# Kernel tuning notes

Hardware: AMD Instinct MI355X
Metric: run time of the kernel (lower is better)

## Reference

```python
import jax, jax.numpy as jnp
import numpy as np

N_PART = 32
DIM = 256
BATCH = 8192
N_TRAIN = 8192
EPS = 1e-8


def rbf_kernel(x):
    # x: [n, d] particles; RBF kernel with median heuristic (Liu & Wang SVGD)
    n = x.shape[0]
    sq = jnp.sum(x * x, axis=1)
    pd = sq[:, None] - 2.0 * (x @ x.T) + sq[None, :]          # [n, n] squared dists
    h = jnp.median(pd) / jnp.log(n + 1.0)                      # bandwidth
    kxy = jnp.exp(-pd / h)                                     # [n, n]
    sumk = jnp.sum(kxy, axis=1)
    # sum_j grad_{x_j} k(x_j, x_i): (x_i * sum_j k_ij - sum_j k_ij x_j) * 2/h
    dxkxy = (x * sumk[:, None] - kxy @ x) * (2.0 / h)          # [n, d]
    return kxy, dxkxy


def setup_inputs() -> dict:
    key = jax.random.key(0)
    k1, k2, k3 = jax.random.split(key, 3)
    X = jax.random.normal(k1, (BATCH, DIM), dtype=jnp.float32)
    y = (jax.random.uniform(k2, (BATCH,), dtype=jnp.float32) > 0.5).astype(jnp.float32)
    W = jax.random.uniform(k3, (N_PART, DIM), dtype=jnp.float32) * 0.2 - 0.1
    return {"X": X, "y": y, "W": W}


def reference(X, y, W):
    z = W @ X.T
    p = jax.nn.sigmoid(z)
    denom = p - p * p + EPS
    # dz * dy, where dy = (y - p)/denom and dz = p(1-p)
    dzdy = (p * (1.0 - p)) * (y[None, :] - p) / denom          # [n, B]
    dW = (dzdy @ X) / BATCH                                     # mean over batch -> [n, d]
    # grad_loglik_W = -(dz*dy)[:, :, None] * X[None]  -> [n, B, d]
    glW = (-dzdy)[:, :, None] * X[None, :, :]
    mean_dW = jnp.mean(glW, axis=0)                             # [B, d]
    diff = glW - mean_dW[None]                                  # [n, B, d]
    # mean over particles of diff^T diff, divided by batch_size
    cov = jnp.einsum('nbd,nbe->de', diff, diff) / (N_PART * BATCH)  # [d, d]
    W_grads = dW * N_TRAIN - W                                  # [n, d]
    y_pred = jnp.mean(p, axis=0)                                # [B]
    ll = jnp.mean(y * jnp.log(y_pred + 1e-3) + (1.0 - y) * jnp.log(1.0 - y_pred + 1e-3))
    acc = jnp.mean(((y > 0.5) == (y_pred > 0.5)).astype(jnp.float32))
    # step == 1 -> rho = 0 -> updated cov buffer equals cov
    H_inv = jnp.linalg.inv(cov + 0.01 * jnp.eye(DIM, dtype=cov.dtype))
    kxy, dxkxy = rbf_kernel(W)
    svgd_grad = (kxy @ W_grads + dxkxy) / N_PART               # [n, d]
    kfac_grad = svgd_grad @ H_inv                               # [n, d]
    return (ll, acc, svgd_grad, kfac_grad)
```

## Files before the change

### kernel.cpp

```cpp
#include <hip/hip_runtime.h>

#define NPART 32
#define DIM   256
#define BATCH 8192

#define OFF_S     0u
#define OFF_DWP   270336u
#define OFF_WG    2367488u
#define OFF_COVP  2375680u
#define OFF_H     6569984u
#define OFF_EA    6635520u
#define OFF_EB    6701056u
#define OFF_XA    6766592u
#define OFF_XB    6832128u
#define OFF_SVGD  6897664u
#define OFF_LLP   6905856u
#define OFF_ACCP  6906368u
#define OFF_TAU   6906624u
#define OFF_KXY   6906628u
#define OFF_SUMK  6907652u
#define OFF_HB    6907684u

__device__ __forceinline__ float dot4(float4 a, float4 b) {
  return a.x*b.x + a.y*b.y + a.z*b.z + a.w*b.w;
}

__global__ __launch_bounds__(512) void k_stage1(
    const float4* __restrict__ X4, const float* __restrict__ y,
    const float* __restrict__ W, float* __restrict__ ws)
{
  __shared__ __align__(16) float smemf[17856];
  const int t = threadIdx.x, blk = blockIdx.x;

  float* s_ws = ws + OFF_S;
  double* llp = (double*)(ws + OFF_LLP);
  float* accp = ws + OFF_ACCP;

  if (blk > 0) {
    float2* Wl2 = (float2*)smemf;
    float4* Xl  = (float4*)(smemf + 8384);
    float*  dzl = smemf + 16704;
    double* llred  = (double*)(smemf + 17760);
    float*  accred = smemf + 17824;
    const int chunk = blk - 1;
    const int base = chunk*32;
    const float4* W4g = (const float4*)W;

    #pragma unroll
    for (int i = 0; i < 4; ++i) {
      int idx = t + i*512;
      float4 v = W4g[idx];
      int n = idx >> 6, j = idx & 63;
      Wl2[n*131 + 2*j]     = make_float2(v.x, v.y);
      Wl2[n*131 + 2*j + 1] = make_float2(v.z, v.w);
    }
    #pragma unroll
    for (int i = 0; i < 4; ++i) {
      int idx = t + i*512;
      Xl[(idx>>6)*65 + (idx&63)] = X4[(base + (idx>>6))*64 + (idx&63)];
    }
    __syncthreads();

    const int n = t & 31, b2 = t >> 5;
    float z0 = 0.f, z1 = 0.f;
    #pragma unroll 8
    for (int c = 0; c < 64; ++c) {
      float2 wa = Wl2[n*131 + 2*c], wb = Wl2[n*131 + 2*c + 1];
      float4 xa = Xl[b2*65 + c], xb = Xl[(b2+16)*65 + c];
      z0 += wa.x*xa.x + wa.y*xa.y + wb.x*xa.z + wb.y*xa.w;
      z1 += wa.x*xb.x + wa.y*xb.y + wb.x*xb.z + wb.y*xb.w;
    }
    const int g0 = base + b2, g1 = base + b2 + 16;
    const float y0 = y[g0], y1 = y[g1];
    float p0 = 1.f/(1.f + expf(-z0)), p1 = 1.f/(1.f + expf(-z1));

    auto dzf = [](float p, float yv) {
      float pq = p - p*p;
      return pq*(yv - p)/(pq + 1e-8f);
    };
    float dz0 = dzf(p0, y0), dz1 = dzf(p1, y1);

    float sp0 = p0, sp1 = p1, sd0 = dz0, sd1 = dz1;
    #pragma unroll
    for (int m = 16; m >= 1; m >>= 1) {
      sp0 += __shfl_xor(sp0, m); sp1 += __shfl_xor(sp1, m);
      sd0 += __shfl_xor(sd0, m); sd1 += __shfl_xor(sd1, m);
    }
    const float m0 = sd0*(1.f/32.f), m1 = sd1*(1.f/32.f);
    float q0 = (dz0 - m0)*(dz0 - m0);
    float q1 = (dz1 - m1)*(dz1 - m1);
    #pragma unroll
    for (int m = 16; m >= 1; m >>= 1) {
      q0 += __shfl_xor(q0, m); q1 += __shfl_xor(q1, m);
    }

    dzl[b2*33 + n]      = dz0;
    dzl[(b2+16)*33 + n] = dz1;

    if (n == 0) {
      s_ws[g0] = q0; s_ws[g1] = q1;
      float yp0 = sp0*(1.f/32.f), yp1 = sp1*(1.f/32.f);
      llred[b2]    = (double)(y0*logf(yp0+1e-3f) + (1.f-y0)*logf(1.f-yp0+1e-3f));
      llred[b2+16] = (double)(y1*logf(yp1+1e-3f) + (1.f-y1)*logf(1.f-yp1+1e-3f));
      accred[b2]    = ((y0 > 0.5f) == (yp0 > 0.5f)) ? 1.f : 0.f;
      accred[b2+16] = ((y1 > 0.5f) == (yp1 > 0.5f)) ? 1.f : 0.f;
    }
    __syncthreads();

    const int n2 = t >> 4, c = t & 15;
    float4 acc[4];
    #pragma unroll
    for (int m = 0; m < 4; ++m) acc[m] = make_float4(0.f,0.f,0.f,0.f);
    #pragma unroll 4
    for (int b = 0; b < 32; ++b) {
      float dzv = dzl[b*33 + n2];
      #pragma unroll
      for (int m = 0; m < 4; ++m) {
        float4 xv = Xl[b*65 + c + 16*m];
        acc[m].x += dzv*xv.x; acc[m].y += dzv*xv.y;
        acc[m].z += dzv*xv.z; acc[m].w += dzv*xv.w;
      }
    }
    float4* dWp4 = (float4*)(ws + OFF_DWP);
    #pragma unroll
    for (int m = 0; m < 4; ++m)
      dWp4[chunk*2048 + n2*64 + c + 16*m] = acc[m];

    if (t == 0) {
      double L = 0.0;
      for (int i = 0; i < 32; ++i) L += llred[i];
      llp[chunk] = L;
    } else if (t == 1) {
      float A = 0.f;
      for (int i = 0; i < 32; ++i) A += accred[i];
      accp[chunk] = A;
    }
  } else {
    if (t == 0) *(unsigned*)(ws + OFF_TAU) = 0u;
    float* Wf = &smemf[0];
    float* pd = &smemf[8320];
    float* sb = &smemf[9344];
    for (int i = t; i < 8192; i += 512)
      Wf[(i>>8)*260 + (i&255)] = W[i];
    __syncthreads();
    for (int pp = t; pp < 1024; pp += 512) {
      int i = pp >> 5, j = pp & 31;
      const float4* wa = (const float4*)&Wf[i*260];
      const float4* wb = (const float4*)&Wf[j*260];
      float d2 = 0.f;
      #pragma unroll 8
      for (int c = 0; c < 64; ++c) {
        float4 a = wa[c], b = wb[c];
        float dx=a.x-b.x, dy=a.y-b.y, dz=a.z-b.z, dw=a.w-b.w;
        d2 += dx*dx + dy*dy + dz*dz + dw*dw;
      }
      pd[pp] = d2; sb[pp] = d2;
    }
    __syncthreads();
    for (int k = 2; k <= 1024; k <<= 1) {
      for (int j = k >> 1; j > 0; j >>= 1) {
        #pragma unroll 1
        for (int m = t; m < 1024; m += 512) {
          int ixj = m ^ j;
          if (ixj > m) {
            float a = sb[m], b = sb[ixj];
            bool up = ((m & k) == 0);
            if ((a > b) == up) { sb[m] = b; sb[ixj] = a; }
          }
        }
        __syncthreads();
      }
    }
    const float h = 0.5f*(sb[511] + sb[512]) / logf(33.0f);
    __syncthreads();
    float* kxy = ws + OFF_KXY;
    for (int pp = t; pp < 1024; pp += 512) {
      float kv = expf(-pd[pp]/h);
      sb[pp] = kv;
      kxy[pp] = kv;
    }
    __syncthreads();
    if (t < 32) {
      float s = 0.f;
      #pragma unroll
      for (int j = 0; j < 32; ++j) s += sb[t*32 + j];
      (ws + OFF_SUMK)[t] = s;
    }
    if (t == 0) (ws + OFF_HB)[0] = h;
  }
}

__global__ __launch_bounds__(256) void k_stage2(
    const float4* __restrict__ X4, const float* __restrict__ W,
    float* __restrict__ out, float* __restrict__ ws)
{
  __shared__ __align__(16) float smemf[8448];
  const int t = threadIdx.x, blk = blockIdx.x;
  float* s_ws = ws + OFF_S;
  float* covp = ws + OFF_COVP;

  if (blk == 0) {
    if (t == 0) {
      const double* llp = (const double*)(ws + OFF_LLP);
      double L = 0.0;
      for (int k = 0; k < 256; ++k) L += llp[k];
      out[0] = (float)(L / 8192.0);
    } else if (t == 1) {
      const float* accp = ws + OFF_ACCP;
      float A = 0.f;
      for (int k = 0; k < 256; ++k) A += accp[k];
      out[1] = A / 8192.f;
    }
  } else if (blk >= 193) {
    const int i = blk - 193;
    const float* dWp = ws + OFF_DWP;
    float sum = 0.f;
    #pragma unroll 8
    for (int k = 0; k < 256; ++k) sum += dWp[k*8192 + i*256 + t];
    (ws + OFF_WG)[i*256 + t] = sum - W[i*256 + t];
  } else {
    const int cb = blk - 1;
    const int p = cb >> 6, z = cb & 63;
    const int pi = (p == 2) ? 1 : 0;
    const int pj = (p == 0) ? 0 : 1;
    float4* Ad = (float4*)smemf;
    float4* Ae = (float4*)(smemf + 4224);
    const int tx = t & 15, ty = t >> 4;
    const int lrow = t >> 5, lc4 = t & 31;
    float acc[8][8];
    #pragma unroll
    for (int i = 0; i < 8; ++i)
      #pragma unroll
      for (int j = 0; j < 8; ++j) acc[i][j] = 0.f;

    float  rsv[4]; float4 rxd[4], rxe[4];
    auto loadsub = [&](int b0) {
      #pragma unroll
      for (int i = 0; i < 4; ++i) {
        int row = lrow + i*8;
        rsv[i] = s_ws[b0+row];
        rxd[i] = X4[(b0+row)*64 + pi*32 + lc4];
        rxe[i] = X4[(b0+row)*64 + pj*32 + lc4];
      }
    };
    loadsub(z*128);
    for (int sub = 0; sub < 4; ++sub) {
      __syncthreads();
      #pragma unroll
      for (int i = 0; i < 4; ++i) {
        int row = lrow + i*8;
        float sv = rsv[i]; float4 xv = rxd[i];
        Ad[row*33 + lc4] = make_float4(xv.x*sv, xv.y*sv, xv.z*sv, xv.w*sv);
        Ae[row*33 + lc4] = rxe[i];
      }
      __syncthreads();
      if (sub < 3) loadsub(z*128 + (sub+1)*32);
      #pragma unroll 2
      for (int b = 0; b < 32; ++b) {
        float4 a0 = Ad[b*33 + tx], a1 = Ad[b*33 + tx + 16];
        float4 e0 = Ae[b*33 + ty], e1 = Ae[b*33 + ty + 16];
        const float av[8] = {a0.x,a0.y,a0.z,a0.w, a1.x,a1.y,a1.z,a1.w};
        const float ev[8] = {e0.x,e0.y,e0.z,e0.w, e1.x,e1.y,e1.z,e1.w};
        #pragma unroll
        for (int i = 0; i < 8; ++i)
          #pragma unroll
          for (int j = 0; j < 8; ++j) acc[i][j] += av[i]*ev[j];
      }
    }
    float* cz = covp + (unsigned)z*65536u;
    float4* cz4 = (float4*)cz;
    #pragma unroll
    for (int ha = 0; ha < 2; ++ha)
      #pragma unroll
      for (int i = 0; i < 4; ++i) {
        const int gd = pi*128 + (tx + 16*ha)*4 + i;
        cz4[gd*64 + pj*32 + ty]      = make_float4(acc[4*ha+i][0], acc[4*ha+i][1], acc[4*ha+i][2], acc[4*ha+i][3]);
        cz4[gd*64 + pj*32 + ty + 16] = make_float4(acc[4*ha+i][4], acc[4*ha+i][5], acc[4*ha+i][6], acc[4*ha+i][7]);
      }
    if (p == 1) {
      #pragma unroll
      for (int he = 0; he < 2; ++he)
        #pragma unroll
        for (int j = 0; j < 4; ++j) {
          const int ge = pj*128 + (ty + 16*he)*4 + j;
          #pragma unroll
          for (int ha = 0; ha < 2; ++ha)
            #pragma unroll
            for (int i = 0; i < 4; ++i)
              cz[ge*256 + pi*128 + (tx + 16*ha)*4 + i] = acc[4*ha+i][4*he+j];
        }
    }
  }
}

__global__ __launch_bounds__(256) void k_stage3(
    const float* __restrict__ W, float* __restrict__ out,
    float* __restrict__ ws)
{
  __shared__ __align__(16) float smemf[8300];
  const int t = threadIdx.x, blk = blockIdx.x;
  float* covp = ws + OFF_COVP;

  if (blk < 256) {
    const int d = blk;
    float sum = 0.f;
    #pragma unroll 8
    for (int z = 0; z < 64; ++z) sum += covp[(unsigned)z*65536u + d*256 + t];
    float h = sum * (1.f/262144.f) + ((d == t) ? 0.01f : 0.f);
    (ws + OFF_H)[d*256 + t] = h;
    float a = fabsf(h);
    #pragma unroll
    for (int m = 32; m >= 1; m >>= 1) a += __shfl_xor(a, m);
    if ((t & 63) == 0) smemf[t >> 6] = a;
    __syncthreads();
    if (t == 0) {
      float r = smemf[0] + smemf[1] + smemf[2] + smemf[3];
      atomicMax((unsigned*)(ws + OFF_TAU), __float_as_uint(r));
    }
  } else {
    const int i = blk - 256;
    float* G   = &smemf[0];
    float* kxr = &smemf[8224];
    const float* Wg = ws + OFF_WG;
    const float h = (ws + OFF_HB)[0];
    const float c2 = 2.f/h;
    for (int idx = t; idx < 8192; idx += 256) {
      int j = idx >> 8, d = idx & 255;
      G[j*257 + d] = Wg[idx] - c2*W[idx];
    }
    if (t < 32) kxr[t] = (ws + OFF_KXY)[i*32 + t];
    __syncthreads();
    float acc = 0.f;
    #pragma unroll 8
    for (int j = 0; j < 32; ++j) acc += kxr[j] * G[j*257 + t];
    float r = (acc + c2*(ws + OFF_SUMK)[i]*W[i*256 + t]) * (1.f/32.f);
    (ws + OFF_SVGD)[i*256 + t] = r;
    out[2 + i*256 + t] = r;
  }
}

__global__ __launch_bounds__(256) void k_ns1(float* __restrict__ ws)
{
  __shared__ __align__(16) float smemf[2176];
  const int t = threadIdx.x, blk = blockIdx.x;
  const float* H = ws + OFF_H;
  const float tau = __uint_as_float(*(const unsigned*)(ws + OFF_TAU));
  const float alpha = 2.f/(tau + 0.01f);

  if (blk < 64) {
    float* At = smemf;
    float* Bs = smemf + 1088;
    const int i0 = (blk >> 3)*32, j0 = (blk & 7)*32;
    const int ti = t & 15, tj = t >> 4;
    const int srow = t >> 3, sc4 = t & 7;
    const float4* H4 = (const float4*)H;
    float acc00=0.f, acc01=0.f, acc10=0.f, acc11=0.f;

    float4 av = H4[(i0+srow)*64 + sc4];
    float4 bv = H4[srow*64 + (j0>>2) + sc4];
    for (int k0 = 0; k0 < 8; ++k0) {
      __syncthreads();
      At[(sc4*4+0)*34+srow]=av.x; At[(sc4*4+1)*34+srow]=av.y;
      At[(sc4*4+2)*34+srow]=av.z; At[(sc4*4+3)*34+srow]=av.w;
      Bs[srow*34+sc4*4+0]=bv.x; Bs[srow*34+sc4*4+1]=bv.y;
      Bs[srow*34+sc4*4+2]=bv.z; Bs[srow*34+sc4*4+3]=bv.w;
      __syncthreads();
      if (k0 < 7) {
        av = H4[(i0+srow)*64 + (k0+1)*8 + sc4];
        bv = H4[((k0+1)*32+srow)*64 + (j0>>2) + sc4];
      }
      #pragma unroll
      for (int kk = 0; kk < 32; ++kk) {
        float2 a = *(const float2*)&At[kk*34+2*ti];
        float2 b = *(const float2*)&Bs[kk*34+2*tj];
        acc00 += a.x*b.x; acc01 += a.x*b.y;
        acc10 += a.y*b.x; acc11 += a.y*b.y;
      }
    }
    const int gi = i0 + 2*ti, gj = j0 + 2*tj;
    float* E1 = ws + OFF_EA;
    const float a2 = alpha*alpha, ta = 2.f*alpha;
    E1[gi*256+gj]       = a2*acc00 - ta*H[gi*256+gj]       + ((gi   == gj  ) ? 1.f : 0.f);
    E1[gi*256+gj+1]     = a2*acc01 - ta*H[gi*256+gj+1]     + ((gi   == gj+1) ? 1.f : 0.f);
    E1[(gi+1)*256+gj]   = a2*acc10 - ta*H[(gi+1)*256+gj]   + ((gi+1 == gj  ) ? 1.f : 0.f);
    E1[(gi+1)*256+gj+1] = a2*acc11 - ta*H[(gi+1)*256+gj+1] + ((gi+1 == gj+1) ? 1.f : 0.f);
  } else {
    float* X1 = ws + OFF_XA;
    #pragma unroll
    for (int rr = 0; rr < 4; ++rr) {
      const int d = (blk - 64)*4 + rr;
      const float h = H[d*256 + t];
      X1[d*256 + t] = alpha*(((d == t) ? 2.f : 0.f) - alpha*h);
    }
  }
}

__global__ __launch_bounds__(1024) void k_kfac(
    const float* __restrict__ E, const float* __restrict__ Xm,
    float* __restrict__ out, float* __restrict__ ws)
{
  __shared__ float sv[256];
  __shared__ float u[256];
  __shared__ float vcur[256];
  __shared__ __align__(16) float part[16][256];
  const int t = threadIdx.x, i = blockIdx.x;
  const int c4 = t & 63, g = t >> 6;

  if (t < 256) sv[t] = (ws + OFF_SVGD)[i*256 + t];
  __syncthreads();

  const float4* E4 = (const float4*)E;
  const float4* Xm4 = (const float4*)Xm;
  float4* partq = (float4*)&part[g][0];

  {
    float4 acc = make_float4(0.f,0.f,0.f,0.f);
    #pragma unroll
    for (int kk = 0; kk < 16; ++kk) {
      const int k = g*16 + kk;
      const float vk = sv[k];
      float4 e = Xm4[k*64 + c4];
      acc.x += vk*e.x; acc.y += vk*e.y; acc.z += vk*e.z; acc.w += vk*e.w;
    }
    partq[c4] = acc;
    __syncthreads();
    if (t < 256) {
      float s = 0.f;
      #pragma unroll
      for (int gg = 0; gg < 16; ++gg) s += part[gg][t];
      u[t] = s; vcur[t] = s;
    }
    __syncthreads();
  }
  for (int pass = 0; pass < 7; ++pass) {
    float4 acc = make_float4(0.f,0.f,0.f,0.f);
    #pragma unroll
    for (int kk = 0; kk < 16; ++kk) {
      const int k = g*16 + kk;
      const float vk = vcur[k];
      float4 e = E4[k*64 + c4];
      acc.x += vk*e.x; acc.y += vk*e.y; acc.z += vk*e.z; acc.w += vk*e.w;
    }
    partq[c4] = acc;
    __syncthreads();
    if (t < 256) {
      float s = u[t];
      #pragma unroll
      for (int gg = 0; gg < 16; ++gg) s += part[gg][t];
      vcur[t] = s;
    }
    __syncthreads();
  }
  if (t < 256) out[2 + 8192 + i*256 + t] = vcur[t];
}

extern "C" void kernel_launch(void* const* d_in, const int* in_sizes, int n_in,
                              void* d_out, int out_size, void* d_ws, size_t ws_size,
                              hipStream_t stream) {
  (void)in_sizes; (void)n_in; (void)out_size; (void)ws_size;
  const float* X = (const float*)d_in[0];
  const float* y = (const float*)d_in[1];
  const float* W = (const float*)d_in[2];
  float* out = (float*)d_out;
  float* ws  = (float*)d_ws;

  float* EA = ws + OFF_EA;
  float* XA = ws + OFF_XA;

  k_stage1<<<257, 512, 0, stream>>>((const float4*)X, y, W, ws);
  k_stage2<<<225, 256, 0, stream>>>((const float4*)X, W, out, ws);
  k_stage3<<<288, 256, 0, stream>>>(W, out, ws);
  k_ns1<<<128, 256, 0, stream>>>(ws);
  k_kfac<<<32, 1024, 0, stream>>>(EA, XA, out, ws);
}
```

Before: 81.62 us.

## Replace Newton-Schulz matrix squaring with direct Richardson iteration on H

Removes the k_ns1 kernel, which formed E=(I-alpha H)^2 with a 256x256 matmul and a scaled X matrix. The k_kfac kernel now runs 15 plain Richardson/Neumann matvec passes directly against H (v = u + v - alpha*H v) instead of 1+7 passes against the squared operator. This saves a kernel launch and the dense matmul, but doubles the number of serial matvec passes per particle block.

```diff
diff --git a/kernel.cpp b/kernel.cpp
--- a/kernel.cpp
+++ b/kernel.cpp
@@ -9,10 +9,6 @@
 #define OFF_WG    2367488u
 #define OFF_COVP  2375680u
 #define OFF_H     6569984u
-#define OFF_EA    6635520u
-#define OFF_EB    6701056u
-#define OFF_XA    6766592u
-#define OFF_XB    6832128u
 #define OFF_SVGD  6897664u
 #define OFF_LLP   6905856u
 #define OFF_ACCP  6906368u
@@ -339,115 +335,44 @@
   }
 }
 
-__global__ __launch_bounds__(256) void k_ns1(float* __restrict__ ws)
+__global__ __launch_bounds__(1024) void k_kfac(
+    const float* __restrict__ H, float* __restrict__ out,
+    float* __restrict__ ws)
 {
-  __shared__ __align__(16) float smemf[2176];
-  const int t = threadIdx.x, blk = blockIdx.x;
-  const float* H = ws + OFF_H;
-  const float tau = __uint_as_float(*(const unsigned*)(ws + OFF_TAU));
-  const float alpha = 2.f/(tau + 0.01f);
-
-  if (blk < 64) {
-    float* At = smemf;
-    float* Bs = smemf + 1088;
-    const int i0 = (blk >> 3)*32, j0 = (blk & 7)*32;
-    const int ti = t & 15, tj = t >> 4;
-    const int srow = t >> 3, sc4 = t & 7;
-    const float4* H4 = (const float4*)H;
-    float acc00=0.f, acc01=0.f, acc10=0.f, acc11=0.f;
-
-    float4 av = H4[(i0+srow)*64 + sc4];
-    float4 bv = H4[srow*64 + (j0>>2) + sc4];
-    for (int k0 = 0; k0 < 8; ++k0) {
-      __syncthreads();
-      At[(sc4*4+0)*34+srow]=av.x; At[(sc4*4+1)*34+srow]=av.y;
-      At[(sc4*4+2)*34+srow]=av.z; At[(sc4*4+3)*34+srow]=av.w;
-      Bs[srow*34+sc4*4+0]=bv.x; Bs[srow*34+sc4*4+1]=bv.y;
-      Bs[srow*34+sc4*4+2]=bv.z; Bs[srow*34+sc4*4+3]=bv.w;
-      __syncthreads();
-      if (k0 < 7) {
-        av = H4[(i0+srow)*64 + (k0+1)*8 + sc4];
-        bv = H4[((k0+1)*32+srow)*64 + (j0>>2) + sc4];
-      }
-      #pragma unroll
-      for (int kk = 0; kk < 32; ++kk) {
-        float2 a = *(const float2*)&At[kk*34+2*ti];
-        float2 b = *(const float2*)&Bs[kk*34+2*tj];
-        acc00 += a.x*b.x; acc01 += a.x*b.y;
-        acc10 += a.y*b.x; acc11 += a.y*b.y;
-      }
-    }
-    const int gi = i0 + 2*ti, gj = j0 + 2*tj;
-    float* E1 = ws + OFF_EA;
-    const float a2 = alpha*alpha, ta = 2.f*alpha;
-    E1[gi*256+gj]       = a2*acc00 - ta*H[gi*256+gj]       + ((gi   == gj  ) ? 1.f : 0.f);
-    E1[gi*256+gj+1]     = a2*acc01 - ta*H[gi*256+gj+1]     + ((gi   == gj+1) ? 1.f : 0.f);
-    E1[(gi+1)*256+gj]   = a2*acc10 - ta*H[(gi+1)*256+gj]   + ((gi+1 == gj  ) ? 1.f : 0.f);
-    E1[(gi+1)*256+gj+1] = a2*acc11 - ta*H[(gi+1)*256+gj+1] + ((gi+1 == gj+1) ? 1.f : 0.f);
-  } else {
-    float* X1 = ws + OFF_XA;
-    #pragma unroll
-    for (int rr = 0; rr < 4; ++rr) {
-      const int d = (blk - 64)*4 + rr;
-      const float h = H[d*256 + t];
-      X1[d*256 + t] = alpha*(((d == t) ? 2.f : 0.f) - alpha*h);
-    }
-  }
-}
-
-__global__ __launch_bounds__(1024) void k_kfac(
-    const float* __restrict__ E, const float* __restrict__ Xm,
-    float* __restrict__ out, float* __restrict__ ws)
-{
-  __shared__ float sv[256];
   __shared__ float u[256];
   __shared__ float vcur[256];
   __shared__ __align__(16) float part[16][256];
   const int t = threadIdx.x, i = blockIdx.x;
   const int c4 = t & 63, g = t >> 6;
 
-  if (t < 256) sv[t] = (ws + OFF_SVGD)[i*256 + t];
+  const float tau = __uint_as_float(*(const unsigned*)(ws + OFF_TAU));
+  const float alpha = 2.f/(tau + 0.01f);
+
+  if (t < 256) {
+    float s = alpha * (ws + OFF_SVGD)[i*256 + t];
+    u[t] = s; vcur[t] = s;
+  }
   __syncthreads();
 
-  const float4* E4 = (const float4*)E;
-  const float4* Xm4 = (const float4*)Xm;
+  const float4* H4 = (const float4*)H;
   float4* partq = (float4*)&part[g][0];
 
-  {
-    float4 acc = make_float4(0.f,0.f,0.f,0.f);
-    #pragma unroll
-    for (int kk = 0; kk < 16; ++kk) {
-      const int k = g*16 + kk;
-      const float vk = sv[k];
-      float4 e = Xm4[k*64 + c4];
-      acc.x += vk*e.x; acc.y += vk*e.y; acc.z += vk*e.z; acc.w += vk*e.w;
-    }
-    partq[c4] = acc;
-    __syncthreads();
-    if (t < 256) {
-      float s = 0.f;
-      #pragma unroll
-      for (int gg = 0; gg < 16; ++gg) s += part[gg][t];
-      u[t] = s; vcur[t] = s;
-    }
-    __syncthreads();
-  }
-  for (int pass = 0; pass < 7; ++pass) {
+  for (int pass = 0; pass < 15; ++pass) {
     float4 acc = make_float4(0.f,0.f,0.f,0.f);
     #pragma unroll
     for (int kk = 0; kk < 16; ++kk) {
       const int k = g*16 + kk;
       const float vk = vcur[k];
-      float4 e = E4[k*64 + c4];
+      float4 e = H4[k*64 + c4];
       acc.x += vk*e.x; acc.y += vk*e.y; acc.z += vk*e.z; acc.w += vk*e.w;
     }
     partq[c4] = acc;
     __syncthreads();
     if (t < 256) {
-      float s = u[t];
-      #pragma unroll
-      for (int gg = 0; gg < 16; ++gg) s += part[gg][t];
-      vcur[t] = s;
+      float w = 0.f;
+      #pragma unroll
+      for (int gg = 0; gg < 16; ++gg) w += part[gg][t];
+      vcur[t] = u[t] + vcur[t] - alpha*w;
     }
     __syncthreads();
   }
@@ -464,12 +389,8 @@
   float* out = (float*)d_out;
   float* ws  = (float*)d_ws;
 
-  float* EA = ws + OFF_EA;
-  float* XA = ws + OFF_XA;
-
   k_stage1<<<257, 512, 0, stream>>>((const float4*)X, y, W, ws);
   k_stage2<<<225, 256, 0, stream>>>((const float4*)X, W, out, ws);
   k_stage3<<<288, 256, 0, stream>>>(W, out, ws);
-  k_ns1<<<128, 256, 0, stream>>>(ws);
-  k_kfac<<<32, 1024, 0, stream>>>(EA, XA, out, ws);
-}
+  k_kfac<<<32, 1024, 0, stream>>>(ws + OFF_H, out, ws);
+}
```

After: 76.61 us. -6.1%, faster.
